# Performance work log

Hardware: AMD Instinct MI355X
Metric: run time of the kernel (lower is better)

The kernel has to match this reference:

```python
import jax, jax.numpy as jnp
import numpy as np

T = 1_000_000  # sequence length
H = 5          # LSTM hidden size
NC = 4         # number of channel streams (all fed through lstm1, as in the original)


def setup_inputs() -> dict:
    key = jax.random.key(0)
    ks = jax.random.split(key, 14)
    s = 1.0 / np.sqrt(H)  # PyTorch default LSTM/Linear init scale
    u = lambda k, shape: jax.random.uniform(k, shape, jnp.float32, -s, s)
    sf1 = 1.0 / np.sqrt(20.0)
    sf2 = 1.0 / np.sqrt(10.0)
    return {
        "inputs": jax.random.normal(ks[0], (T, 1, NC), jnp.float32),
        # lstm1 layer 0: input_size=1
        "w_ih0": u(ks[1], (4 * H, 1)),
        "w_hh0": u(ks[2], (4 * H, H)),
        "b_ih0": u(ks[3], (4 * H,)),
        "b_hh0": u(ks[4], (4 * H,)),
        # lstm1 layer 1: input_size=H
        "w_ih1": u(ks[5], (4 * H, H)),
        "w_hh1": u(ks[6], (4 * H, H)),
        "b_ih1": u(ks[7], (4 * H,)),
        "b_hh1": u(ks[8], (4 * H,)),
        "fc1_w": jax.random.uniform(ks[9], (10, 20), jnp.float32, -sf1, sf1),
        "fc1_b": jax.random.uniform(ks[10], (10,), jnp.float32, -sf1, sf1),
        "fc2_w": jax.random.uniform(ks[11], (1, 10), jnp.float32, -sf2, sf2),
        "fc2_b": jax.random.uniform(ks[12], (1,), jnp.float32, -sf2, sf2),
    }


def _lstm_layer(x_seq, w_ih, w_hh, b_ih, b_hh):
    """Single PyTorch-style LSTM layer. x_seq: (T, B, in) -> h_seq: (T, B, H)."""
    # Input projection for all timesteps at once (outside the scan).
    gx = jnp.einsum('tbi,gi->tbg', x_seq, w_ih) + b_ih + b_hh  # (T, B, 4H)

    def step(carry, gx_t):
        h, c = carry
        g = gx_t + h @ w_hh.T                      # (B, 4H)
        i, f, gg, o = jnp.split(g, 4, axis=-1)     # PyTorch gate order i,f,g,o
        i = jax.nn.sigmoid(i)
        f = jax.nn.sigmoid(f)
        gg = jnp.tanh(gg)
        o = jax.nn.sigmoid(o)
        c = f * c + i * gg
        h = o * jnp.tanh(c)
        return (h, c), h

    B = x_seq.shape[1]
    z = jnp.zeros((B, H), x_seq.dtype)
    _, h_seq = jax.lax.scan(step, (z, z), gx)
    return h_seq


def reference(inputs, w_ih0, w_hh0, b_ih0, b_hh0, w_ih1, w_hh1, b_ih1, b_hh1,
              fc1_w, fc1_b, fc2_w, fc2_b):
    # Original code runs all 4 channel streams through lstm1 (lstm2-4 unused),
    # so we fold the 4 streams into the LSTM batch dim: (T, 4, 1).
    x = inputs[:, 0, :, None]                      # (T, NC, 1)
    h = _lstm_layer(x, w_ih0, w_hh0, b_ih0, b_hh0)  # (T, NC, H)
    h = _lstm_layer(h, w_ih1, w_hh1, b_ih1, b_hh1)  # (T, NC, H)
    # torch.cat((out1..out4), dim=2) on (T,1,H) slices == channel-major reshape
    out_cat = h.reshape(T, 1, NC * H)              # (T, 1, 20)
    out = out_cat @ fc1_w.T + fc1_b                # (T, 1, 10)
    out = out @ fc2_w.T + fc2_b                    # (T, 1, 1)
    return out
```

## Files before the change

### kernel.cpp

```cpp
#include <hip/hip_runtime.h>

#define T_TOTAL 1000000
#define NCHUNK  12288
#define CLEN    82
#define WARM    24


typedef float v2 __attribute__((ext_vector_type(2)));

#define L2E  1.44269504088896340736f
#define K2   2.88539008177792681472f

__device__ __forceinline__ float bperm(int addr4, float v) {
    return __int_as_float(__builtin_amdgcn_ds_bpermute(addr4, __float_as_int(v)));
}
__device__ __forceinline__ v2 pkfma(v2 a, v2 b, v2 c) {
    return __builtin_elementwise_fma(a, b, c);
}

__global__ __launch_bounds__(64, 1) void lstm_chunks(
    const float* __restrict__ inp,
    const float* __restrict__ wih0,
    const float* __restrict__ whh0,
    const float* __restrict__ bih0,
    const float* __restrict__ bhh0,
    const float* __restrict__ wih1,
    const float* __restrict__ whh1,
    const float* __restrict__ bih1,
    const float* __restrict__ bhh1,
    const float* __restrict__ fc1w,
    const float* __restrict__ fc1b,
    const float* __restrict__ fc2w,
    const float* __restrict__ fc2b,
    float* __restrict__ out)
{
    const int lane = threadIdx.x & 63;
    int cw = lane / 20; if (cw > 2) cw = 2;
    int q  = lane - cw * 20; if (q > 19) q = 19;
    const int b = q / 5;
    const int j = q % 5;
    const int chunk = blockIdx.x * 3 + cw;
    const int base  = cw * 20;

    int gh[5];
    #pragma unroll
    for (int k = 0; k < 5; ++k) gh[k] = (base + b * 5 + k) * 4;
    const int rd5  = (lane + 5)  * 4;
    const int rd10 = (lane + 10) * 4;

    v2 W0x01, W0x23, BB001, BB023, BB101, BB123;
    v2 W0h01[5], W0h23[5], W1a01[5], W1a23[5], W1b01[5], W1b23[5];
    {
        const int r0 = j, r1 = 5 + j, r2 = 10 + j, r3 = 15 + j;
        const v2 s01 = v2{-L2E, -L2E};
        const v2 s23 = v2{-K2,  -L2E};
        W0x01 = s01 * v2{wih0[r0], wih0[r1]};
        W0x23 = s23 * v2{wih0[r2], wih0[r3]};
        BB001 = s01 * v2{bih0[r0] + bhh0[r0], bih0[r1] + bhh0[r1]};
        BB023 = s23 * v2{bih0[r2] + bhh0[r2], bih0[r3] + bhh0[r3]};
        BB101 = s01 * v2{bih1[r0] + bhh1[r0], bih1[r1] + bhh1[r1]};
        BB123 = s23 * v2{bih1[r2] + bhh1[r2], bih1[r3] + bhh1[r3]};
        #pragma unroll
        for (int k = 0; k < 5; ++k) {
            W0h01[k] = s01 * v2{whh0[r0 * 5 + k], whh0[r1 * 5 + k]};
            W0h23[k] = s23 * v2{whh0[r2 * 5 + k], whh0[r3 * 5 + k]};
            W1a01[k] = s01 * v2{wih1[r0 * 5 + k], wih1[r1 * 5 + k]};
            W1a23[k] = s23 * v2{wih1[r2 * 5 + k], wih1[r3 * 5 + k]};
            W1b01[k] = s01 * v2{whh1[r0 * 5 + k], whh1[r1 * 5 + k]};
            W1b23[k] = s23 * v2{whh1[r2 * 5 + k], whh1[r3 * 5 + k]};
        }
    }
    float vb[5] = {0, 0, 0, 0, 0};
    float sc = fc2b[0];
    #pragma unroll
    for (int m = 0; m < 10; ++m) {
        const float f2 = fc2w[m];
        sc = __builtin_fmaf(f2, fc1b[m], sc);
        #pragma unroll
        for (int k = 0; k < 5; ++k)
            vb[k] = __builtin_fmaf(f2, fc1w[m * 20 + b * 5 + k], vb[k]);
    }

    const int o_begin = chunk * CLEN;
    const int warm = (chunk == 0) ? 0 : WARM;

    float C0 = 0.0f, C1 = 0.0f;
    float h0r[5] = {0, 0, 0, 0, 0};
    float h1r[5] = {0, 0, 0, 0, 0};

    auto ldx = [&](int t) -> float {
        const int tt = (t > T_TOTAL - 1) ? (T_TOTAL - 1) : t;
        return inp[(size_t)tt * 4 + b];
    };

    auto cellp = [&](v2 A01, v2 A23, float& C) -> float {
        const float ei = __builtin_amdgcn_exp2f(A01.x);
        const float ef = __builtin_amdgcn_exp2f(A01.y);
        const float eg = __builtin_amdgcn_exp2f(A23.x);
        const float eo = __builtin_amdgcn_exp2f(A23.y);
        const float Di = 1.0f + ei, Df = 1.0f + ef, Dg = 1.0f + eg, Do = 1.0f + eo;
        const float p1 = Di * Df, p2 = Dg * Do, p3 = Df * Do;
        const float r  = __builtin_amdgcn_rcpf(p1 * p2);
        const float f  = (Di * p2) * r;
        const float o  = (p1 * Dg) * r;
        const float tg = __builtin_fmaf(K2, eg, -K2);
        C = __builtin_fmaf(f, C, (tg * p3) * r);
        const float eh = __builtin_amdgcn_exp2f(C);
        return (o * (1.0f - eh)) * __builtin_amdgcn_rcpf(1.0f + eh);
    };

    auto matvec0 = [&](float x, const float (&h)[5], v2& A01, v2& A23) {
        const v2 xx = v2{x, x};
        v2 P01 = pkfma(W0x01, xx, BB001);
        v2 P23 = pkfma(W0x23, xx, BB023);
        const v2 k0 = v2{h[0], h[0]}, k1 = v2{h[1], h[1]};
        const v2 k2 = v2{h[2], h[2]}, k3 = v2{h[3], h[3]};
        const v2 k4 = v2{h[4], h[4]};
        P01 = pkfma(W0h01[0], k0, P01);  v2 Q01 = W0h01[2] * k2;
        P23 = pkfma(W0h23[0], k0, P23);  v2 Q23 = W0h23[2] * k2;
        P01 = pkfma(W0h01[1], k1, P01);  Q01 = pkfma(W0h01[3], k3, Q01);
        P23 = pkfma(W0h23[1], k1, P23);  Q23 = pkfma(W0h23[3], k3, Q23);
        Q01 = pkfma(W0h01[4], k4, Q01);
        Q23 = pkfma(W0h23[4], k4, Q23);
        A01 = P01 + Q01; A23 = P23 + Q23;
    };
    auto matvec1 = [&](const float (&h0)[5], const float (&h1)[5], v2& A01, v2& A23) {
        v2 P01 = BB101, P23 = BB123;
        const v2 g0 = v2{h1[0], h1[0]};
        v2 Q01 = W1b01[0] * g0;
        v2 Q23 = W1b23[0] * g0;
        #pragma unroll
        for (int k = 0; k < 5; ++k) {
            const v2 hk = v2{h0[k], h0[k]};
            P01 = pkfma(W1a01[k], hk, P01);
            P23 = pkfma(W1a23[k], hk, P23);
        }
        #pragma unroll
        for (int k = 1; k < 5; ++k) {
            const v2 gk = v2{h1[k], h1[k]};
            Q01 = pkfma(W1b01[k], gk, Q01);
            Q23 = pkfma(W1b23[k], gk, Q23);
        }
        A01 = P01 + Q01; A23 = P23 + Q23;
    };

    int t = o_begin - warm;
    {
        v2 A01, A23;
        matvec0(ldx(t), h0r, A01, A23);
        const float h0 = cellp(A01, A23, C0);
        #pragma unroll
        for (int k = 0; k < 5; ++k) h0r[k] = bperm(gh[k], h0);
    }
    float xc = ldx(t + 1);

    #define BODY(EMIT)                                                         \
    {                                                                          \
        v2 A01, A23;                                                           \
        matvec1(h0r, h1r, A01, A23);                                           \
        const float h1 = cellp(A01, A23, C1);                                  \
        float h1n[5];                                                          \
        _Pragma("unroll")                                                      \
        for (int k = 0; k < 5; ++k) h1n[k] = bperm(gh[k], h1);                 \
        const float xn = ldx(t + 2);                                           \
        matvec0(xc, h0r, A01, A23);                                            \
        const float h0 = cellp(A01, A23, C0);                                  \
        _Pragma("unroll")                                                      \
        for (int k = 0; k < 5; ++k) h0r[k] = bperm(gh[k], h0);                 \
        xc = xn;                                                               \
        if (EMIT) {                                                            \
            float p = vb[0] * h1n[0];                                          \
            p = __builtin_fmaf(vb[1], h1n[1], p);                              \
            p = __builtin_fmaf(vb[2], h1n[2], p);                              \
            p = __builtin_fmaf(vb[3], h1n[3], p);                              \
            p = __builtin_fmaf(vb[4], h1n[4], p);                              \
            const float u = p + bperm(rd5, p);                                 \
            const float S = u + bperm(rd10, u);                                \
            if (q == 0 && t < T_TOTAL) out[t] = S + sc;                        \
        }                                                                      \
        _Pragma("unroll")                                                      \
        for (int k = 0; k < 5; ++k) h1r[k] = h1n[k];                           \
    }

    for (int i = 0; i < warm; ++i, ++t) BODY(false)
    for (int i = 0; i < CLEN; ++i, ++t) BODY(true)

    #undef BODY
}

extern "C" void kernel_launch(void* const* d_in, const int* in_sizes, int n_in,
                              void* d_out, int out_size, void* d_ws, size_t ws_size,
                              hipStream_t stream) {
    (void)in_sizes; (void)n_in; (void)d_ws; (void)ws_size; (void)out_size;
    lstm_chunks<<<NCHUNK / 3, 64, 0, stream>>>(
        (const float*)d_in[0],  (const float*)d_in[1],  (const float*)d_in[2],
        (const float*)d_in[3],  (const float*)d_in[4],  (const float*)d_in[5],
        (const float*)d_in[6],  (const float*)d_in[7],  (const float*)d_in[8],
        (const float*)d_in[9],  (const float*)d_in[10], (const float*)d_in[11],
        (const float*)d_in[12], (float*)d_out);
}
```

Measured before the change: 186.5 us.

## Halve chunk count with longer chunks and ping-pong h1 buffers

Halves the number of time chunks and doubles chunk length, so each wave runs fewer warmup steps relative to useful output and there are fewer total redundant warmup recurrences. The step loop is unrolled by two with ping-pong h1 register arrays to drop the per-step copy. The trade-off is longer serial chains per wave and fewer waves (2048 blocks), which lowers latency hiding and occupancy on the GPU.

After: 185.9 us. No clear change (-0.3%).

```diff
diff --git a/kernel.cpp b/kernel.cpp
--- a/kernel.cpp
+++ b/kernel.cpp
@@ -1,8 +1,8 @@
 #include <hip/hip_runtime.h>
 
 #define T_TOTAL 1000000
-#define NCHUNK  12288
-#define CLEN    82
+#define NCHUNK  6144
+#define CLEN    163
 #define WARM    24
 
 
@@ -86,10 +86,11 @@
 
     float C0 = 0.0f, C1 = 0.0f;
     float h0r[5] = {0, 0, 0, 0, 0};
-    float h1r[5] = {0, 0, 0, 0, 0};
-
-    auto ldx = [&](int t) -> float {
-        const int tt = (t > T_TOTAL - 1) ? (T_TOTAL - 1) : t;
+    float h1A[5] = {0, 0, 0, 0, 0};
+    float h1B[5] = {0, 0, 0, 0, 0};
+
+    auto ldx = [&](int t_) -> float {
+        const int tt = (t_ > T_TOTAL - 1) ? (T_TOTAL - 1) : t_;
         return inp[(size_t)tt * 4 + b];
     };
 
@@ -154,14 +155,13 @@
     }
     float xc = ldx(t + 1);
 
-    #define BODY(EMIT)                                                         \
+    #define STEP(H1IN, H1OUT, EMIT)                                            \
     {                                                                          \
         v2 A01, A23;                                                           \
-        matvec1(h0r, h1r, A01, A23);                                           \
+        matvec1(h0r, H1IN, A01, A23);                                          \
         const float h1 = cellp(A01, A23, C1);                                  \
-        float h1n[5];                                                          \
         _Pragma("unroll")                                                      \
-        for (int k = 0; k < 5; ++k) h1n[k] = bperm(gh[k], h1);                 \
+        for (int k = 0; k < 5; ++k) H1OUT[k] = bperm(gh[k], h1);               \
         const float xn = ldx(t + 2);                                           \
         matvec0(xc, h0r, A01, A23);                                            \
         const float h0 = cellp(A01, A23, C0);                                  \
@@ -169,23 +169,23 @@
         for (int k = 0; k < 5; ++k) h0r[k] = bperm(gh[k], h0);                 \
         xc = xn;                                                               \
         if (EMIT) {                                                            \
-            float p = vb[0] * h1n[0];                                          \
-            p = __builtin_fmaf(vb[1], h1n[1], p);                              \
-            p = __builtin_fmaf(vb[2], h1n[2], p);                              \
-            p = __builtin_fmaf(vb[3], h1n[3], p);                              \
-            p = __builtin_fmaf(vb[4], h1n[4], p);                              \
+            float p = vb[0] * H1OUT[0];                                        \
+            p = __builtin_fmaf(vb[1], H1OUT[1], p);                            \
+            p = __builtin_fmaf(vb[2], H1OUT[2], p);                            \
+            p = __builtin_fmaf(vb[3], H1OUT[3], p);                            \
+            p = __builtin_fmaf(vb[4], H1OUT[4], p);                            \
             const float u = p + bperm(rd5, p);                                 \
             const float S = u + bperm(rd10, u);                                \
             if (q == 0 && t < T_TOTAL) out[t] = S + sc;                        \
         }                                                                      \
-        _Pragma("unroll")                                                      \
-        for (int k = 0; k < 5; ++k) h1r[k] = h1n[k];                           \
-    }
-
-    for (int i = 0; i < warm; ++i, ++t) BODY(false)
-    for (int i = 0; i < CLEN; ++i, ++t) BODY(true)
-
-    #undef BODY
+        ++t;                                                                   \
+    }
+
+    for (int i = 0; i < warm; i += 2) { STEP(h1A, h1B, false) STEP(h1B, h1A, false) }
+    for (int i = 0; i < CLEN - 1; i += 2) { STEP(h1A, h1B, true) STEP(h1B, h1A, true) }
+    STEP(h1A, h1B, true)
+
+    #undef STEP
 }
 
 extern "C" void kernel_launch(void* const* d_in, const int* in_sizes, int n_in,
```
